# Kernel optimization log

Hardware: AMD Instinct MI355X
Metric: run time of the kernel (lower is better)

Reference implementation:

```python
import jax, jax.numpy as jnp
import numpy as np
from jax import lax

SIM_RATIO = 0.5
TAU = 1e-4
BN_EPS = 1e-5
COS_EPS = 1e-6
LEAKY_SLOPE = 0.01


def setup_inputs() -> dict:
    key = jax.random.key(0)
    ks = jax.random.split(key, 4)
    B, N, D = 2048, 50000, 128
    user_item_id = jax.random.randint(ks[0], (B, 2), 0, N, dtype=jnp.int64 if jax.config.jax_enable_x64 else jnp.int32).astype(jnp.int32)
    item_feature = jax.random.normal(ks[1], (B, 2 * D), dtype=jnp.float32)
    all_items = jax.random.normal(ks[2], (N, D), dtype=jnp.float32)
    # Linear(2D -> D) params (stored transposed: x @ W + b), BatchNorm1d affine params
    W = jax.random.normal(ks[3], (2 * D, D), dtype=jnp.float32) / np.float32(np.sqrt(2 * D))
    b = jnp.zeros((D,), jnp.float32)
    gamma = jnp.ones((D,), jnp.float32)
    beta = jnp.zeros((D,), jnp.float32)
    return {"user_item_id": user_item_id, "item_feature": item_feature,
            "all_items": all_items, "W": W, "b": b, "gamma": gamma, "beta": beta}


def _mlp(x, W, b, gamma, beta):
    # Linear + BatchNorm1d (training mode: batch stats, biased var) + LeakyReLU
    h = x @ W + b                                  # [B, D]
    mean = h.mean(axis=0)
    var = ((h - mean) ** 2).mean(axis=0)
    h = (h - mean) * lax.rsqrt(var + BN_EPS) * gamma + beta
    return jnp.where(h >= 0, h, LEAKY_SLOPE * h)


def reference(user_item_id, item_feature, all_items, W, b, gamma, beta):
    B = item_feature.shape[0]
    N = all_items.shape[0]
    h = _mlp(item_feature, W, b, gamma, beta)       # [B, D]
    scores = h @ all_items.T                         # [B, N]
    # hard gumbel-softmax, tau=1e-4
    g = jax.random.gumbel(jax.random.key(42), scores.shape, scores.dtype)
    soft = jax.nn.softmax((scores + g) / TAU, axis=-1)
    idx = jnp.argmax(soft, axis=-1)                  # [B]
    onehot = jax.nn.one_hot(idx, N, dtype=scores.dtype)
    probs = onehot + soft - lax.stop_gradient(soft)  # straight-through hard one-hot
    repl_feat = probs @ all_items                    # [B, D] (one-hot gather via matmul)
    repl_items = (jnp.arange(N, dtype=scores.dtype) * probs).sum(axis=1).astype(jnp.int32)
    orig_feat = all_items[user_item_id[:, 1]]        # [B, D]
    # cosine similarity along dim=1 with eps=1e-6 (torch semantics)
    dot = (orig_feat * repl_feat).sum(axis=1)
    n1 = jnp.maximum(jnp.linalg.norm(orig_feat, axis=1), COS_EPS)
    n2 = jnp.maximum(jnp.linalg.norm(repl_feat, axis=1), COS_EPS)
    sim = dot / (n1 * n2)
    sim = (sim + 1.0) / 2.0                          # regularize_similarity
    labels = jnp.full((B,), SIM_RATIO, dtype=sim.dtype)
    sim_loss = jnp.mean((sim - labels) ** 2)         # SimilarityMarginLoss ~ MSE to ratio
    return repl_items, sim_loss, sim.mean()
```

## Files before the change

kernel.cpp:

```cpp
#include <hip/hip_runtime.h>
#include <math.h>

#define TINYF 1.17549435e-38f
#define GMAX 16.0f
#define NTILES 1563
#define TPB 25

typedef __attribute__((ext_vector_type(8))) short bf16x8;
typedef __attribute__((ext_vector_type(4))) float f32x4;

__device__ __forceinline__ unsigned rotl32(unsigned x, int r) {
  return (x << r) | (x >> (32 - r));
}

__device__ __forceinline__ unsigned tf2x32_xor(unsigned x0, unsigned x1) {
  const unsigned k0 = 0u, k1 = 42u, k2 = 0x1BD11BF0u;
  x0 += k0; x1 += k1;
#define TFR(r) { x0 += x1; x1 = rotl32(x1, r); x1 ^= x0; }
  TFR(13) TFR(15) TFR(26) TFR(6)
  x0 += k1; x1 += k2 + 1u;
  TFR(17) TFR(29) TFR(16) TFR(24)
  x0 += k2; x1 += k0 + 2u;
  TFR(13) TFR(15) TFR(26) TFR(6)
  x0 += k0; x1 += k1 + 3u;
  TFR(17) TFR(29) TFR(16) TFR(24)
  x0 += k1; x1 += k2 + 4u;
  TFR(13) TFR(15) TFR(26) TFR(6)
  x0 += k2; x1 += k0 + 5u;
#undef TFR
  return x0 ^ x1;
}

__device__ __forceinline__ float gumbel_from_bits(unsigned bits) {
  float f = __uint_as_float((bits >> 9) | 0x3f800000u) - 1.0f;
  float u = fmaxf(f, TINYF);
  return -logf(-logf(u));
}

__device__ __forceinline__ unsigned ordf(float v) {
  unsigned b = __float_as_uint(v);
  return (b & 0x80000000u) ? ~b : (b | 0x80000000u);
}
__device__ __forceinline__ float unordf(unsigned u) {
  unsigned b = (u & 0x80000000u) ? (u & 0x7FFFFFFFu) : ~u;
  return __uint_as_float(b);
}

__device__ __forceinline__ unsigned short f2bf(float f) {
  unsigned u = __float_as_uint(f);
  unsigned r = u + 0x7FFFu + ((u >> 16) & 1u);
  return (unsigned short)(r >> 16);
}
__device__ __forceinline__ unsigned pk2(float a, float b) {
  return (unsigned)f2bf(a) | ((unsigned)f2bf(b) << 16);
}
__device__ __forceinline__ int bswz(int b) { return b ^ (((b >> 8) & 7) << 4); }

__device__ __attribute__((noinline)) void resolve_cand(
    int R, int J, float s, float ERRC,
    const float* __restrict__ hfin, const float* __restrict__ items,
    const float* __restrict__ V0,
    unsigned long long* __restrict__ rowslot, const volatile unsigned* hiw) {
  const unsigned hi0 = hiw[2 * R + 1];
  float tv = V0[R];
  if (hi0) tv = fmaxf(tv, unordf(hi0));
  const float thr2 = tv - ERRC;
  const float d = thr2 - s;
  const unsigned bits = tf2x32_xor(0u, (unsigned)R * 50000u + (unsigned)J);
  const float f = __uint_as_float((bits >> 9) | 0x3f800000u) - 1.0f;
  const float u = fmaxf(f, TINYF);
  const float thr_u = __expf(-__expf(-d)) * (1.0f - 2e-5f);
  if (u < thr_u) return;
  const float g = -logf(-logf(u));
  if (s + g < thr2) return;
  const float4* hp = (const float4*)(hfin + (size_t)R * 128);
  const float4* ap = (const float4*)(items + (size_t)J * 128);
  float4 a4 = {0.f, 0.f, 0.f, 0.f};
#pragma unroll
  for (int k = 0; k < 32; ++k) {
    float4 h = hp[k];
    float4 b = ap[k];
    a4.x = fmaf(h.x, b.x, a4.x);
    a4.y = fmaf(h.y, b.y, a4.y);
    a4.z = fmaf(h.z, b.z, a4.z);
    a4.w = fmaf(h.w, b.w, a4.w);
  }
  const float v = ((a4.x + a4.y) + (a4.z + a4.w)) + g;
  const unsigned ov = ordf(v);
  if (ov >= hiw[2 * R + 1]) {
    const unsigned long long pk =
        ((unsigned long long)ov << 32) | (0xFFFFFFFFu - (unsigned)J);
    atomicMax(&rowslot[R], pk);
  }
}

__global__ void k_hraw(const float* __restrict__ x, const float* __restrict__ W,
                       const float* __restrict__ b, float* __restrict__ hraw,
                       unsigned long long* __restrict__ rowslot,
                       float* __restrict__ norms) {
  __shared__ float sx[256];
  const int i = blockIdx.x;
  const int d = threadIdx.x;
  if (d == 0) {
    rowslot[i] = 0ull;
    if (i == 0) { norms[0] = 0.0f; norms[1] = 0.0f; }
  }
  sx[d] = x[i * 256 + d];
  sx[d + 128] = x[i * 256 + 128 + d];
  __syncthreads();
  double acc = 0.0;
  for (int k = 0; k < 256; ++k)
    acc = fma((double)sx[k], (double)W[k * 128 + d], acc);
  hraw[i * 128 + d] = (float)acc + b[d];
}

__global__ void k_bca(const float* __restrict__ items,
                      unsigned short* __restrict__ ib,
                      float* __restrict__ norms) {
  __shared__ float red[4];
  const int t = threadIdx.x;
  const int row = blockIdx.x * 32 + (t >> 3);
  const int rc = row > 49999 ? 49999 : row;
  const int c = (t & 7) * 16;
  const float4* p = (const float4*)(items + (size_t)rc * 128 + c);
  const float4 v0 = p[0], v1 = p[1], v2 = p[2], v3 = p[3];
  float ss = v0.x * v0.x + v0.y * v0.y + v0.z * v0.z + v0.w * v0.w +
             v1.x * v1.x + v1.y * v1.y + v1.z * v1.z + v1.w * v1.w +
             v2.x * v2.x + v2.y * v2.y + v2.z * v2.z + v2.w * v2.w +
             v3.x * v3.x + v3.y * v3.y + v3.z * v3.z + v3.w * v3.w;
  if (row <= 49999) {
    uint4 o0, o1;
    o0.x = pk2(v0.x, v0.y); o0.y = pk2(v0.z, v0.w);
    o0.z = pk2(v1.x, v1.y); o0.w = pk2(v1.z, v1.w);
    o1.x = pk2(v2.x, v2.y); o1.y = pk2(v2.z, v2.w);
    o1.z = pk2(v3.x, v3.y); o1.w = pk2(v3.z, v3.w);
    uint4* dst = (uint4*)(ib + (size_t)row * 128 + c);
    dst[0] = o0; dst[1] = o1;
  }
  ss += __shfl_xor(ss, 1);
  ss += __shfl_xor(ss, 2);
  ss += __shfl_xor(ss, 4);
  ss = fmaxf(ss, __shfl_xor(ss, 8));
  ss = fmaxf(ss, __shfl_xor(ss, 16));
  ss = fmaxf(ss, __shfl_xor(ss, 32));
  if ((t & 63) == 0) red[t >> 6] = ss;
  __syncthreads();
  if (t == 0) {
    float mx = fmaxf(fmaxf(red[0], red[1]), fmaxf(red[2], red[3]));
    atomicMax((unsigned*)&norms[1], __float_as_uint(mx));
  }
}

__global__ void k_bnstats(const float* __restrict__ hraw,
                          float* __restrict__ meanv, float* __restrict__ rsv) {
  __shared__ double red[256];
  const int d = blockIdx.x;
  const int t = threadIdx.x;
  double s = 0.0;
  for (int i = t; i < 2048; i += 256) s += (double)hraw[i * 128 + d];
  red[t] = s;
  __syncthreads();
  for (int off = 128; off > 0; off >>= 1) {
    if (t < off) red[t] += red[t + off];
    __syncthreads();
  }
  const float m = (float)(red[0] * (1.0 / 2048.0));
  __syncthreads();
  double v = 0.0;
  for (int i = t; i < 2048; i += 256) {
    float dd = __fsub_rn(hraw[i * 128 + d], m);
    v += (double)dd * (double)dd;
  }
  red[t] = v;
  __syncthreads();
  for (int off = 128; off > 0; off >>= 1) {
    if (t < off) red[t] += red[t + off];
    __syncthreads();
  }
  if (t == 0) {
    float var = (float)(red[0] * (1.0 / 2048.0));
    float vpe = __fadd_rn(var, 1e-5f);
    meanv[d] = m;
    rsv[d] = (float)(1.0 / sqrt((double)vpe));
  }
}

__global__ void k_apply(const float* __restrict__ hraw,
                        const float* __restrict__ meanv, const float* __restrict__ rsv,
                        const float* __restrict__ gamma, const float* __restrict__ beta,
                        float* __restrict__ hfin, unsigned short* __restrict__ hb,
                        float* __restrict__ norms) {
  __shared__ float red[256];
  const int t = threadIdx.x;
  const int idx = blockIdx.x * 256 + t;
  const int d = idx & 127;
  float h = hraw[idx];
  float hn = __fadd_rn(__fmul_rn(__fmul_rn(__fsub_rn(h, meanv[d]), rsv[d]), gamma[d]), beta[d]);
  float o = (hn >= 0.0f) ? hn : __fmul_rn(0.01f, hn);
  hfin[idx] = o;
  hb[idx] = f2bf(o);
  red[t] = o * o;
  __syncthreads();
  for (int off = 64; off > 0; off >>= 1) {
    if ((t & 127) < off) red[t] += red[t + off];
    __syncthreads();
  }
  if ((t & 127) == 0) atomicMax((unsigned*)&norms[0], __float_as_uint(red[t]));
}

__global__ __launch_bounds__(256, 4) void k_seed(const float* __restrict__ hfin,
                                                 const float* __restrict__ items,
                                                 float* __restrict__ V0) {
  __shared__ float red[4][256];
  const int t = threadIdx.x;
  const int rbase = blockIdx.x * 4;
  float best[4] = {-INFINITY, -INFINITY, -INFINITY, -INFINITY};
  for (int q = 0; q < 4; ++q) {
    const int j = t + 256 * q;
    float acc[4] = {0.0f, 0.0f, 0.0f, 0.0f};
    const float* ap = items + (size_t)j * 128;
    for (int km = 0; km < 8; ++km) {
#pragma unroll
      for (int e = 0; e < 4; ++e) {
        float4 a4 = *(const float4*)(ap + km * 16 + 4 * e);
#pragma unroll
        for (int p = 0; p < 4; ++p) {
          const float* hp = hfin + (rbase + p) * 128 + km * 16 + 4 * e;
          float4 h4 = *(const float4*)hp;
          acc[p] = fmaf(h4.x, a4.x, acc[p]);
          acc[p] = fmaf(h4.y, a4.y, acc[p]);
          acc[p] = fmaf(h4.z, a4.z, acc[p]);
          acc[p] = fmaf(h4.w, a4.w, acc[p]);
        }
      }
    }
#pragma unroll
    for (int p = 0; p < 4; ++p) {
      unsigned l = (unsigned)(rbase + p) * 50000u + (unsigned)j;
      float g = gumbel_from_bits(tf2x32_xor(0u, l));
      best[p] = fmaxf(best[p], acc[p] + g);
    }
  }
#pragma unroll
  for (int p = 0; p < 4; ++p) red[p][t] = best[p];
  __syncthreads();
  for (int off = 128; off > 0; off >>= 1) {
    if (t < off) {
#pragma unroll
      for (int p = 0; p < 4; ++p) red[p][t] = fmaxf(red[p][t], red[p][t + off]);
    }
    __syncthreads();
  }
  if (t < 4) V0[rbase + t] = red[t][0];
}

__global__ __launch_bounds__(256, 2) void k_screen(
    const unsigned short* __restrict__ hb, const float* __restrict__ hfin,
    const float* __restrict__ items, const unsigned short* __restrict__ ib,
    const float* __restrict__ V0,
    const float* __restrict__ norms, unsigned long long* __restrict__ rowslot) {
  __shared__ __align__(16) unsigned short Bs[2][32 * 128];
  __shared__ unsigned qk[4][128];
  __shared__ float qsh[4][128];

  const int t = threadIdx.x;
  const int w = t >> 6, l = t & 63;
  const int lg = l >> 4, lr = l & 15;
  const int rg = blockIdx.x >> 6;
  const int span = blockIdx.x & 63;
  const int r0w = rg * 64 + w * 16;
  const int tile0 = span * TPB;
  int nt = NTILES - tile0;
  nt = nt < 0 ? 0 : (nt > TPB ? TPB : nt);
  if (nt == 0) return;

  const float ERRC = 0.004f * sqrtf(norms[0] * norms[1]) + 0.01f;
  const volatile unsigned* hiw = (const volatile unsigned*)rowslot;

  const unsigned short* aB0 = hb + (size_t)(r0w + lr) * 128 + lg * 8;
  bf16x8 Afrag[4];
#pragma unroll
  for (int kb = 0; kb < 4; ++kb) Afrag[kb] = *(const bf16x8*)(aB0 + kb * 32);

  const int o0 = w * 2048 + l * 16;
  const int row0 = o0 >> 8, col0 = o0 & 255;
  const int o1 = o0 + 1024;
  const int row1 = o1 >> 8, col1 = o1 & 255;
  const int sc0 = col0 ^ ((row0 & 7) << 4);
  const int sc1 = col1 ^ ((row1 & 7) << 4);

#define STAGE_TILE(tl, buf)                                                    \
  {                                                                            \
    const int Jg0 = min((tl) * 32 + row0, 49999);                              \
    const int Jg1 = min((tl) * 32 + row1, 49999);                              \
    __builtin_amdgcn_global_load_lds(                                          \
        (const unsigned int*)((const char*)ib + (size_t)Jg0 * 256 + sc0),      \
        (unsigned int*)((char*)Bs[buf] + w * 2048), 16, 0, 0);                 \
    __builtin_amdgcn_global_load_lds(                                          \
        (const unsigned int*)((const char*)ib + (size_t)Jg1 * 256 + sc1),      \
        (unsigned int*)((char*)Bs[buf] + w * 2048 + 1024), 16, 0, 0);          \
  }

  STAGE_TILE(tile0, 0)
  __syncthreads();

  const unsigned long long lml = (1ull << l) - 1ull;
  unsigned qn = 0;

  int pb = 0;
  for (int it = 0; it < nt; ++it) {
    const int j0 = (tile0 + it) * 32;

    if (it + 1 < nt) STAGE_TILE(tile0 + it + 1, pb ^ 1)

    float tvl = 0.0f;
    if (l < 16) {
      const int R = r0w + l;
      const unsigned hi = hiw[2 * R + 1];
      tvl = V0[R];
      if (hi) tvl = fmaxf(tvl, unordf(hi));
    }
    float th1[4];
#pragma unroll
    for (int q = 0; q < 4; ++q)
      th1[q] = __shfl(tvl, lg * 4 + q) - GMAX - ERRC;

    f32x4 acc[2];
    acc[0] = (f32x4){0.f, 0.f, 0.f, 0.f};
    acc[1] = (f32x4){0.f, 0.f, 0.f, 0.f};
#pragma unroll
    for (int kb = 0; kb < 4; ++kb) {
#pragma unroll
      for (int jt = 0; jt < 2; ++jt) {
        const int byte = (jt * 16 + lr) * 256 + kb * 64 + lg * 16;
        bf16x8 bfrag = *(const bf16x8*)((char*)Bs[pb] + bswz(byte));
        acc[jt] = __builtin_amdgcn_mfma_f32_16x16x32_bf16(Afrag[kb], bfrag, acc[jt], 0, 0, 0);
      }
    }

#pragma unroll
    for (int q = 0; q < 4; ++q) {
      const float th = th1[q];
#pragma unroll
      for (int jt = 0; jt < 2; ++jt) {
        const float s = acc[jt][q];
        const int J = j0 + jt * 16 + lr;
        const bool c = (J < 50000) && (s >= th);
        const unsigned long long m = __ballot(c);
        if (m) {
          if (c) {
            const unsigned idx = qn + (unsigned)__popcll(m & lml);
            qk[w][idx] = ((unsigned)(lg * 4 + q) << 16) | (unsigned)J;
            qsh[w][idx] = s;
          }
          qn += (unsigned)__popcll(m);
          if (qn >= 64) {
            for (unsigned i = (unsigned)l; i < qn; i += 64) {
              const unsigned key = qk[w][i];
              resolve_cand(r0w + (int)(key >> 16), (int)(key & 0xFFFFu),
                           qsh[w][i], ERRC, hfin, items, V0, rowslot, hiw);
            }
            qn = 0;
          }
        }
      }
    }

    __syncthreads();
    pb ^= 1;
  }

  for (unsigned i = (unsigned)l; i < qn; i += 64) {
    const unsigned key = qk[w][i];
    resolve_cand(r0w + (int)(key >> 16), (int)(key & 0xFFFFu),
                 qsh[w][i], ERRC, hfin, items, V0, rowslot, hiw);
  }
#undef STAGE_TILE
}

__global__ void k_final(const unsigned long long* __restrict__ rowslot,
                        const int* __restrict__ uid, const float* __restrict__ items,
                        float* __restrict__ dout, float* __restrict__ simv) {
  const int r = blockIdx.x;
  const int lane = threadIdx.x;
  const unsigned long long pk = rowslot[r];
  const int bi = (int)(0xFFFFFFFFu - (unsigned)pk);
  if (lane == 0) dout[r] = (float)bi;

  const int orig = uid[r * 2 + 1];
  float o1 = items[(size_t)orig * 128 + lane];
  float o2 = items[(size_t)orig * 128 + 64 + lane];
  float p1 = items[(size_t)bi * 128 + lane];
  float p2 = items[(size_t)bi * 128 + 64 + lane];
  float d = o1 * p1 + o2 * p2;
  float s1 = o1 * o1 + o2 * o2;
  float s2 = p1 * p1 + p2 * p2;
  for (int off = 32; off > 0; off >>= 1) {
    d += __shfl_down(d, off);
    s1 += __shfl_down(s1, off);
    s2 += __shfl_down(s2, off);
  }
  if (lane == 0) {
    float n1 = fmaxf(sqrtf(s1), 1e-6f);
    float n2 = fmaxf(sqrtf(s2), 1e-6f);
    float sim = d / (n1 * n2);
    simv[r] = (sim + 1.0f) * 0.5f;
  }
}

__global__ void k_reduce(const float* __restrict__ simv, float* __restrict__ dout) {
  __shared__ double rl[256];
  __shared__ double rs[256];
  const int t = threadIdx.x;
  double L = 0.0, S = 0.0;
  for (int i = t; i < 2048; i += 256) {
    double s = (double)simv[i];
    double dd = s - 0.5;
    L += dd * dd;
    S += s;
  }
  rl[t] = L; rs[t] = S;
  __syncthreads();
  for (int off = 128; off > 0; off >>= 1) {
    if (t < off) { rl[t] += rl[t + off]; rs[t] += rs[t + off]; }
    __syncthreads();
  }
  if (t == 0) {
    dout[2048] = (float)(rl[0] * (1.0 / 2048.0));
    dout[2049] = (float)(rs[0] * (1.0 / 2048.0));
  }
}

extern "C" void kernel_launch(void* const* d_in, const int* in_sizes, int n_in,
                              void* d_out, int out_size, void* d_ws, size_t ws_size,
                              hipStream_t stream) {
  const int* uid = (const int*)d_in[0];
  const float* xfeat = (const float*)d_in[1];
  const float* items = (const float*)d_in[2];
  const float* W = (const float*)d_in[3];
  const float* bias = (const float*)d_in[4];
  const float* gamma = (const float*)d_in[5];
  const float* beta = (const float*)d_in[6];

  float* ws = (float*)d_ws;
  float* hraw = ws;
  float* hfin = ws + 262144;
  float* meanv = ws + 524288;
  float* rsv = ws + 524416;
  float* V0 = ws + 524544;
  float* simv = ws + 526592;
  float* norms = ws + 528640;
  unsigned long long* rowslot =
      (unsigned long long*)(ws + 528642);
  unsigned short* hb = (unsigned short*)(ws + 532740);
  unsigned short* ib = (unsigned short*)(ws + 663812);
  float* dout = (float*)d_out;

  hipLaunchKernelGGL(k_hraw, dim3(2048), dim3(128), 0, stream, xfeat, W, bias, hraw, rowslot, norms);
  hipLaunchKernelGGL(k_bca, dim3(1563), dim3(256), 0, stream, items, ib, norms);
  hipLaunchKernelGGL(k_bnstats, dim3(128), dim3(256), 0, stream, hraw, meanv, rsv);
  hipLaunchKernelGGL(k_apply, dim3(1024), dim3(256), 0, stream, hraw, meanv, rsv, gamma, beta, hfin, hb, norms);
  hipLaunchKernelGGL(k_seed, dim3(512), dim3(256), 0, stream, hfin, items, V0);
  hipLaunchKernelGGL(k_screen, dim3(2048), dim3(256), 0, stream, hb, hfin, items, ib, V0, norms, rowslot);
  hipLaunchKernelGGL(k_final, dim3(2048), dim3(64), 0, stream, rowslot, uid, items, dout, simv);
  hipLaunchKernelGGL(k_reduce, dim3(1), dim3(256), 0, stream, simv, dout);
}
```

Measured before the change: 407.2 us.

## Stage item tiles per wave with vmcnt waits instead of block barriers

The screening kernel now gives each wave its own double-buffered 16-item LDS tile, loaded with four global_load_lds ops per lane. It waits on vmcnt counters rather than a block-wide __syncthreads, so the four waves no longer lockstep. The per-row threshold is refreshed only every 8 tiles instead of every tile. This cuts barrier and threshold-read overhead, but each wave now loads the same item tiles redundantly (four times the LDS-fill traffic), and the staler threshold may let more candidates through. The J<50000 bound check was dropped because 3125 tiles of 16 cover exactly 50000 items.

Measured after the change: 376.6 us. 7.5% less time.

```diff
diff --git a/kernel.cpp b/kernel.cpp
--- a/kernel.cpp
+++ b/kernel.cpp
@@ -3,8 +3,8 @@
 
 #define TINYF 1.17549435e-38f
 #define GMAX 16.0f
-#define NTILES 1563
-#define TPB 25
+#define NT16 3125
+#define SPT16 49
 
 typedef __attribute__((ext_vector_type(8))) short bf16x8;
 typedef __attribute__((ext_vector_type(4))) float f32x4;
@@ -259,7 +259,7 @@
     const float* __restrict__ items, const unsigned short* __restrict__ ib,
     const float* __restrict__ V0,
     const float* __restrict__ norms, unsigned long long* __restrict__ rowslot) {
-  __shared__ __align__(16) unsigned short Bs[2][32 * 128];
+  __shared__ __align__(16) unsigned short Bs[4][2][16 * 128];
   __shared__ unsigned qk[4][128];
   __shared__ float qsh[4][128];
 
@@ -269,9 +269,9 @@
   const int rg = blockIdx.x >> 6;
   const int span = blockIdx.x & 63;
   const int r0w = rg * 64 + w * 16;
-  const int tile0 = span * TPB;
-  int nt = NTILES - tile0;
-  nt = nt < 0 ? 0 : (nt > TPB ? TPB : nt);
+  const int tile0 = span * SPT16;
+  int nt = NT16 - tile0;
+  nt = nt < 0 ? 0 : (nt > SPT16 ? SPT16 : nt);
   if (nt == 0) return;
 
   const float ERRC = 0.004f * sqrtf(norms[0] * norms[1]) + 0.01f;
@@ -282,91 +282,96 @@
 #pragma unroll
   for (int kb = 0; kb < 4; ++kb) Afrag[kb] = *(const bf16x8*)(aB0 + kb * 32);
 
-  const int o0 = w * 2048 + l * 16;
-  const int row0 = o0 >> 8, col0 = o0 & 255;
-  const int o1 = o0 + 1024;
-  const int row1 = o1 >> 8, col1 = o1 & 255;
-  const int sc0 = col0 ^ ((row0 & 7) << 4);
-  const int sc1 = col1 ^ ((row1 & 7) << 4);
-
-#define STAGE_TILE(tl, buf)                                                    \
+  char* wlds = (char*)Bs + w * 8192;
+  const char* ibc = (const char*)ib;
+  int so[4];
+#pragma unroll
+  for (int c = 0; c < 4; ++c) {
+    const int row = c * 4 + (l >> 4);
+    const int col = (l & 15) * 16;
+    so[c] = row * 256 + (col ^ ((row & 7) << 4));
+  }
+
+#define ISSUE(tl, pbuf)                                                        \
   {                                                                            \
-    const int Jg0 = min((tl) * 32 + row0, 49999);                              \
-    const int Jg1 = min((tl) * 32 + row1, 49999);                              \
-    __builtin_amdgcn_global_load_lds(                                          \
-        (const unsigned int*)((const char*)ib + (size_t)Jg0 * 256 + sc0),      \
-        (unsigned int*)((char*)Bs[buf] + w * 2048), 16, 0, 0);                 \
-    __builtin_amdgcn_global_load_lds(                                          \
-        (const unsigned int*)((const char*)ib + (size_t)Jg1 * 256 + sc1),      \
-        (unsigned int*)((char*)Bs[buf] + w * 2048 + 1024), 16, 0, 0);          \
-  }
-
-  STAGE_TILE(tile0, 0)
-  __syncthreads();
+    const char* gs = ibc + (size_t)(tl) * 4096;                                \
+    char* ld = wlds + (pbuf) * 4096;                                           \
+    __builtin_amdgcn_global_load_lds((const unsigned*)(gs + so[0]),            \
+                                     (unsigned*)(ld), 16, 0, 0);               \
+    __builtin_amdgcn_global_load_lds((const unsigned*)(gs + so[1]),            \
+                                     (unsigned*)(ld + 1024), 16, 0, 0);        \
+    __builtin_amdgcn_global_load_lds((const unsigned*)(gs + so[2]),            \
+                                     (unsigned*)(ld + 2048), 16, 0, 0);        \
+    __builtin_amdgcn_global_load_lds((const unsigned*)(gs + so[3]),            \
+                                     (unsigned*)(ld + 3072), 16, 0, 0);        \
+  }
+#define WAITVM4() { asm volatile("s_waitcnt vmcnt(4)" ::: "memory"); \
+                    __builtin_amdgcn_sched_barrier(0); }
+#define WAITVM0() { asm volatile("s_waitcnt vmcnt(0)" ::: "memory"); \
+                    __builtin_amdgcn_sched_barrier(0); }
+
+  ISSUE(tile0, 0)
 
   const unsigned long long lml = (1ull << l) - 1ull;
   unsigned qn = 0;
+  float th1[4];
 
   int pb = 0;
   for (int it = 0; it < nt; ++it) {
-    const int j0 = (tile0 + it) * 32;
-
-    if (it + 1 < nt) STAGE_TILE(tile0 + it + 1, pb ^ 1)
-
-    float tvl = 0.0f;
-    if (l < 16) {
-      const int R = r0w + l;
-      const unsigned hi = hiw[2 * R + 1];
-      tvl = V0[R];
-      if (hi) tvl = fmaxf(tvl, unordf(hi));
-    }
-    float th1[4];
-#pragma unroll
-    for (int q = 0; q < 4; ++q)
-      th1[q] = __shfl(tvl, lg * 4 + q) - GMAX - ERRC;
-
-    f32x4 acc[2];
-    acc[0] = (f32x4){0.f, 0.f, 0.f, 0.f};
-    acc[1] = (f32x4){0.f, 0.f, 0.f, 0.f};
+    const int j0 = (tile0 + it) * 16;
+
+    if (it + 1 < nt) {
+      ISSUE(tile0 + it + 1, pb ^ 1)
+      WAITVM4()
+    } else {
+      WAITVM0()
+    }
+
+    if ((it & 7) == 0) {
+      float tvl = 0.0f;
+      if (l < 16) {
+        const int R = r0w + l;
+        const unsigned hi = hiw[2 * R + 1];
+        tvl = V0[R];
+        if (hi) tvl = fmaxf(tvl, unordf(hi));
+      }
+#pragma unroll
+      for (int q = 0; q < 4; ++q)
+        th1[q] = __shfl(tvl, lg * 4 + q) - GMAX - ERRC;
+    }
+
+    f32x4 acc = (f32x4){0.f, 0.f, 0.f, 0.f};
+    const char* tb = wlds + pb * 4096;
 #pragma unroll
     for (int kb = 0; kb < 4; ++kb) {
-#pragma unroll
-      for (int jt = 0; jt < 2; ++jt) {
-        const int byte = (jt * 16 + lr) * 256 + kb * 64 + lg * 16;
-        bf16x8 bfrag = *(const bf16x8*)((char*)Bs[pb] + bswz(byte));
-        acc[jt] = __builtin_amdgcn_mfma_f32_16x16x32_bf16(Afrag[kb], bfrag, acc[jt], 0, 0, 0);
-      }
+      bf16x8 bfrag = *(const bf16x8*)(tb + bswz(lr * 256 + kb * 64 + lg * 16));
+      acc = __builtin_amdgcn_mfma_f32_16x16x32_bf16(Afrag[kb], bfrag, acc, 0, 0, 0);
     }
 
 #pragma unroll
     for (int q = 0; q < 4; ++q) {
-      const float th = th1[q];
-#pragma unroll
-      for (int jt = 0; jt < 2; ++jt) {
-        const float s = acc[jt][q];
-        const int J = j0 + jt * 16 + lr;
-        const bool c = (J < 50000) && (s >= th);
-        const unsigned long long m = __ballot(c);
-        if (m) {
-          if (c) {
-            const unsigned idx = qn + (unsigned)__popcll(m & lml);
-            qk[w][idx] = ((unsigned)(lg * 4 + q) << 16) | (unsigned)J;
-            qsh[w][idx] = s;
+      const float s = acc[q];
+      const int J = j0 + lr;
+      const bool c = (s >= th1[q]);
+      const unsigned long long m = __ballot(c);
+      if (m) {
+        if (c) {
+          const unsigned idx = qn + (unsigned)__popcll(m & lml);
+          qk[w][idx] = ((unsigned)(lg * 4 + q) << 16) | (unsigned)J;
+          qsh[w][idx] = s;
+        }
+        qn += (unsigned)__popcll(m);
+        if (qn >= 64) {
+          for (unsigned i = (unsigned)l; i < qn; i += 64) {
+            const unsigned key = qk[w][i];
+            resolve_cand(r0w + (int)(key >> 16), (int)(key & 0xFFFFu),
+                         qsh[w][i], ERRC, hfin, items, V0, rowslot, hiw);
           }
-          qn += (unsigned)__popcll(m);
-          if (qn >= 64) {
-            for (unsigned i = (unsigned)l; i < qn; i += 64) {
-              const unsigned key = qk[w][i];
-              resolve_cand(r0w + (int)(key >> 16), (int)(key & 0xFFFFu),
-                           qsh[w][i], ERRC, hfin, items, V0, rowslot, hiw);
-            }
-            qn = 0;
-          }
+          qn = 0;
         }
       }
     }
 
-    __syncthreads();
     pb ^= 1;
   }
 
@@ -375,7 +380,9 @@
     resolve_cand(r0w + (int)(key >> 16), (int)(key & 0xFFFFu),
                  qsh[w][i], ERRC, hfin, items, V0, rowslot, hiw);
   }
-#undef STAGE_TILE
+#undef ISSUE
+#undef WAITVM4
+#undef WAITVM0
 }
 
 __global__ void k_final(const unsigned long long* __restrict__ rowslot,
```
